# Performance work log

Measured on AMD Instinct MI355X. Metric: run time of the kernel, lower is better.

## Reference

```python
import jax, jax.numpy as jnp
import numpy as np

N, D, H, O, E, K = 4096, 512, 1024, 512, 8, 2


def setup_inputs() -> dict:
    key = jax.random.key(0)
    ks = jax.random.split(key, 7)
    s = 0.02
    return {
        "x": jax.random.normal(ks[0], (N, D), dtype=jnp.float32),
        "W1": jax.random.normal(ks[1], (E, D, H), dtype=jnp.float32) * s,
        "b1": jnp.zeros((E, H), dtype=jnp.float32),
        "W2": jax.random.normal(ks[2], (E, H, O), dtype=jnp.float32) * s,
        "b2": jnp.zeros((E, O), dtype=jnp.float32),
        "Wg": jax.random.normal(ks[3], (D, E), dtype=jnp.float32) * s,
        "bg": jnp.zeros((E,), dtype=jnp.float32),
        "k": K,
    }


def reference(x, W1, b1, W2, b2, Wg, bg, k):
    # Gating: softmax over experts, then top-k with renormalized weights
    gates = jax.nn.softmax(x @ Wg + bg, axis=1)              # [N, E]
    topv, topi = jax.lax.top_k(gates, k)                     # [N, k]
    w = topv / jnp.sum(topv, axis=1, keepdims=True)          # renormalized top-k weights

    # Dense per-expert two-layer MLP (grouped GEMM form)
    h = jax.nn.relu(jnp.einsum('nd,edh->neh', x, W1) + b1[None])   # [N, E, H]
    y = jnp.einsum('neh,eho->neo', h, W2) + b2[None]               # [N, E, O]

    # Gather selected experts and combine
    y_sel = jnp.take_along_axis(y, topi[:, :, None], axis=1)       # [N, k, O]
    out = jnp.einsum('nko,nk->no', y_sel, w)                       # [N, O]
    return out, gates, topi
```

## Files before the change

### kernel.cpp

```cpp
#include <hip/hip_runtime.h>
#include <hip/hip_bf16.h>

#define N_TOK 4096
#define DIM   512
#define HID   1024
#define OUTD  512
#define NEXP  8
#define TOPK  2

#define MT1 72
#define HROWS 9216

typedef __bf16 bf16;
typedef bf16  bf16x8 __attribute__((ext_vector_type(8)));
typedef bf16  bf16x4 __attribute__((ext_vector_type(4)));
typedef float f32x4  __attribute__((ext_vector_type(4)));

__device__ inline f32x4 mfma16(bf16x8 a, bf16x8 b, f32x4 c) {
    return __builtin_amdgcn_mfma_f32_16x16x32_bf16(a, b, c, 0, 0, 0);
}

__device__ inline void gload16(const bf16* g, char* l) {
    __builtin_amdgcn_global_load_lds(
        (const __attribute__((address_space(1))) void*)g,
        (__attribute__((address_space(3))) void*)l, 16, 0, 0);
}

__global__ __launch_bounds__(256) void prep_gate_kernel(
    const float* __restrict__ W1, const float* __restrict__ W2,
    const float* __restrict__ Wg, const float* __restrict__ bg,
    const float* __restrict__ x,
    bf16* __restrict__ W1t, bf16* __restrict__ W2t,
    bf16* __restrict__ xb,
    float* __restrict__ gates_out, float* __restrict__ topi_out,
    int* __restrict__ pick_e, float* __restrict__ pick_w)
{
    __shared__ __align__(16) float smem[NEXP * DIM];
    int b = blockIdx.x;

    if (b >= 8192) {
        const float4* Wg4 = (const float4*)Wg;
        for (int i = threadIdx.x; i < DIM * NEXP / 4; i += 256) {
            float4 v = Wg4[i];
#pragma unroll
            for (int j = 0; j < 4; ++j) {
                int idx = i * 4 + j;
                smem[(idx & 7) * DIM + (idx >> 3)] = ((const float*)&v)[j];
            }
        }
        __syncthreads();

        int wave = threadIdx.x >> 6;
        int lane = threadIdx.x & 63;
        int n = (b - 8192) * 4 + wave;

        const float4* x4 = (const float4*)(x + (size_t)n * DIM);
        float4 v0 = x4[lane];
        float4 v1 = x4[lane + 64];

        bf16x4 o0 = { (bf16)v0.x, (bf16)v0.y, (bf16)v0.z, (bf16)v0.w };
        bf16x4 o1 = { (bf16)v1.x, (bf16)v1.y, (bf16)v1.z, (bf16)v1.w };
        bf16x4* xb4 = (bf16x4*)(xb + (size_t)n * DIM);
        xb4[lane]      = o0;
        xb4[lane + 64] = o1;

        float acc[NEXP];
#pragma unroll
        for (int e = 0; e < NEXP; ++e) {
            const float4* wr = (const float4*)(smem + e * DIM);
            float4 w0 = wr[lane];
            float4 w1 = wr[lane + 64];
            acc[e] = v0.x * w0.x + v0.y * w0.y + v0.z * w0.z + v0.w * w0.w
                   + v1.x * w1.x + v1.y * w1.y + v1.z * w1.z + v1.w * w1.w;
        }
#pragma unroll
        for (int off = 32; off >= 1; off >>= 1) {
#pragma unroll
            for (int e = 0; e < NEXP; ++e) acc[e] += __shfl_xor(acc[e], off, 64);
        }
#pragma unroll
        for (int e = 0; e < NEXP; ++e) acc[e] += bg[e];

        float m = acc[0];
#pragma unroll
        for (int e = 1; e < NEXP; ++e) m = fmaxf(m, acc[e]);
        float g[NEXP];
        float s = 0.f;
#pragma unroll
        for (int e = 0; e < NEXP; ++e) { g[e] = expf(acc[e] - m); s += g[e]; }
        float inv_s = 1.f / s;
#pragma unroll
        for (int e = 0; e < NEXP; ++e) g[e] *= inv_s;

        if (lane < NEXP) gates_out[n * NEXP + lane] = g[lane];

        if (lane == 0) {
            int m1 = 0;
#pragma unroll
            for (int e = 1; e < NEXP; ++e) if (g[e] > g[m1]) m1 = e;
            int m2 = (m1 == 0) ? 1 : 0;
#pragma unroll
            for (int e = 0; e < NEXP; ++e) if (e != m1 && g[e] > g[m2]) m2 = e;
            float v1g = g[m1], v2g = g[m2];
            float inv = 1.f / (v1g + v2g);
            topi_out[n * TOPK + 0] = (float)m1;
            topi_out[n * TOPK + 1] = (float)m2;
            int2 pe = { m1, m2 };
            float2 pw = { v1g * inv, v2g * inv };
            *(int2*)(pick_e + n * 2) = pe;
            *(float2*)(pick_w + n * 2) = pw;
        }
        return;
    }

    float (*tile)[33] = (float(*)[33])smem;
    const float* src; bf16* dst; int R, C, tilex, rem, e;
    if (b < 4096) {
        e = b >> 9; rem = b & 511; R = DIM; C = HID; tilex = 32;
        src = W1; dst = W1t;
    } else {
        b -= 4096;
        e = b >> 9; rem = b & 511; R = HID; C = OUTD; tilex = 16;
        src = W2; dst = W2t;
    }
    const float* s = src + (size_t)e * R * C;
    bf16* d = dst + (size_t)e * R * C;
    int c0 = (rem % tilex) * 32, r0 = (rem / tilex) * 32;

    int tx = threadIdx.x & 31, ty = threadIdx.x >> 5;
#pragma unroll
    for (int i = 0; i < 4; ++i) {
        int r = ty + i * 8;
        tile[r][tx] = s[(size_t)(r0 + r) * C + c0 + tx];
    }
    __syncthreads();

    int t = threadIdx.x;
    int dc = t >> 3, q = t & 7;
    bf16x4 v;
#pragma unroll
    for (int j = 0; j < 4; ++j) v[j] = (bf16)tile[q * 4 + j][dc];
    *(bf16x4*)(d + (size_t)(c0 + dc) * R + r0 + q * 4) = v;
}

__global__ __launch_bounds__(1024) void bucket_sched_kernel(
    const int* __restrict__ pick_e,
    int* __restrict__ counts, int* __restrict__ tlist, int* __restrict__ meta)
{
    __shared__ int cnt[NEXP];
    if (threadIdx.x < NEXP) cnt[threadIdx.x] = 0;
    __syncthreads();
    for (int i = threadIdx.x; i < N_TOK * 2; i += 1024) {
        int e = pick_e[i];
        int p = atomicAdd(&cnt[e], 1);
        tlist[e * N_TOK + p] = i;
    }
    __syncthreads();
    if (threadIdx.x == 0) {
        int base = 0, t1 = 0;
        for (int e = 0; e < NEXP; ++e) {
            int c = cnt[e];
            counts[e] = c;
            int n1 = (c + 127) >> 7;
            for (int lt = 0; lt < n1; ++lt) {
                meta[2 + t1 * 3]     = e;
                meta[2 + t1 * 3 + 1] = base + lt * 128;
                meta[2 + t1 * 3 + 2] = lt * 128;
                ++t1;
            }
            base += n1 << 7;
        }
        meta[0] = t1;
    }
}


__global__ __launch_bounds__(256, 4) void l1_kernel(
    const bf16* __restrict__ xb, const bf16* __restrict__ W1t,
    const float* __restrict__ b1, const int* __restrict__ counts,
    const int* __restrict__ tlist, const int* __restrict__ meta,
    bf16* __restrict__ h)
{
    int mt = blockIdx.x >> 3, nt = blockIdx.x & 7;
    if (mt >= meta[0]) return;
    const int* s1 = meta + 2 + mt * 3;
    int e = s1[0], rb = s1[1], i0 = s1[2];
    int cnt = counts[e];

    __shared__ __align__(16) char lds[32768];

    int tid = threadIdx.x, w = tid >> 6, l = tid & 63;
    int c0 = w * 128 + l, c1 = c0 + 64;
    int rA0 = c0 >> 2, rA1 = c1 >> 2;
    int kA0 = (c0 & 3) ^ ((rA0 & 3) ^ ((rA0 >> 2) & 1));
    int kA1 = (c1 & 3) ^ ((rA1 & 3) ^ ((rA1 >> 2) & 1));
    int iA0 = i0 + rA0, iA1 = i0 + rA1;
    const int* tl = tlist + e * N_TOK;
    int tok0 = iA0 < cnt ? (tl[iA0] >> 1) : 0;
    int tok1 = iA1 < cnt ? (tl[iA1] >> 1) : 0;
    const bf16* sA0 = xb + (size_t)tok0 * DIM + kA0 * 8;
    const bf16* sA1 = xb + (size_t)tok1 * DIM + kA1 * 8;
    int n0 = nt * 128;
    const bf16* w1e = W1t + (size_t)e * HID * DIM;
    const bf16* sB0 = w1e + (size_t)(n0 + rA0) * DIM + kA0 * 8;
    const bf16* sB1 = w1e + (size_t)(n0 + rA1) * DIM + kA1 * 8;
    int oA0 = c0 * 16, oA1 = c1 * 16;

    f32x4 acc[4][4];
#pragma unroll
    for (int mf = 0; mf < 4; ++mf)
#pragma unroll
        for (int nf = 0; nf < 4; ++nf) acc[mf][nf] = (f32x4){0.f, 0.f, 0.f, 0.f};

    int wm = w >> 1, wn = w & 1;
    int lr = l & 15;
    int kb = ((l >> 4) ^ ((l & 3) ^ ((l >> 2) & 1))) * 16;

    {
        char* A = lds;       char* B = lds + 8192;
        gload16(sA0, A + oA0); gload16(sA1, A + oA1);
        gload16(sB0, B + oA0); gload16(sB1, B + oA1);
    }

    for (int ks = 0; ks < 16; ++ks) {
        __syncthreads();
        if (ks < 15) {
            char* A = lds + (((ks + 1) & 1) * 16384);
            char* B = A + 8192;
            int kof = (ks + 1) * 32;
            gload16(sA0 + kof, A + oA0); gload16(sA1 + kof, A + oA1);
            gload16(sB0 + kof, B + oA0); gload16(sB1 + kof, B + oA1);
        }
        char* A = lds + ((ks & 1) * 16384);
        char* B = A + 8192;
        bf16x8 af[4], bfr[4];
#pragma unroll
        for (int mf = 0; mf < 4; ++mf)
            af[mf] = *(const bf16x8*)(A + (wm * 64 + mf * 16 + lr) * 64 + kb);
#pragma unroll
        for (int nf = 0; nf < 4; ++nf)
            bfr[nf] = *(const bf16x8*)(B + (wn * 64 + nf * 16 + lr) * 64 + kb);
#pragma unroll
        for (int mf = 0; mf < 4; ++mf)
#pragma unroll
            for (int nf = 0; nf < 4; ++nf)
                acc[mf][nf] = mfma16(af[mf], bfr[nf], acc[mf][nf]);
    }

    __syncthreads();
    bf16* ct = (bf16*)lds;
    const float* b1e = b1 + e * HID;
#pragma unroll
    for (int nf = 0; nf < 4; ++nf) {
        int col = wn * 64 + nf * 16 + lr;
        float bias = b1e[n0 + col];
#pragma unroll
        for (int mf = 0; mf < 4; ++mf) {
#pragma unroll
            for (int r = 0; r < 4; ++r) {
                int row = wm * 64 + mf * 16 + (l >> 4) * 4 + r;
                float v = fmaxf(acc[mf][nf][r] + bias, 0.f);
                int g = (col >> 3) ^ (row & 3);
                ct[row * 128 + g * 8 + (col & 7)] = (bf16)v;
            }
        }
    }
    __syncthreads();
#pragma unroll
    for (int p = 0; p < 8; ++p) {
        int row = p * 16 + (tid >> 4);
        int ch = tid & 15;
        int g = ch ^ (row & 3);
        bf16x8 v = *(const bf16x8*)(ct + row * 128 + g * 8);
        *(bf16x8*)(h + (size_t)(rb + row) * HID + n0 + ch * 8) = v;
    }
}

__global__ __launch_bounds__(256, 4) void l2_kernel(
    const bf16* __restrict__ h, const bf16* __restrict__ W2t,
    const int* __restrict__ counts, const int* __restrict__ tlist,
    const int* __restrict__ meta, bf16* __restrict__ ybuf)
{
    int mt = blockIdx.x >> 2, nt = blockIdx.x & 3;
    if (mt >= meta[0]) return;
    const int* s1 = meta + 2 + mt * 3;
    int e = s1[0], rb = s1[1], i0 = s1[2];
    int cnt = counts[e];

    __shared__ __align__(16) char lds[32768];

    int tid = threadIdx.x, w = tid >> 6, l = tid & 63;
    int c0 = w * 128 + l, c1 = c0 + 64;
    int rA0 = c0 >> 2, rA1 = c1 >> 2;
    int kA0 = (c0 & 3) ^ ((rA0 & 3) ^ ((rA0 >> 2) & 1));
    int kA1 = (c1 & 3) ^ ((rA1 & 3) ^ ((rA1 >> 2) & 1));
    const bf16* sA0 = h + (size_t)(rb + rA0) * HID + kA0 * 8;
    const bf16* sA1 = h + (size_t)(rb + rA1) * HID + kA1 * 8;
    int n0 = nt * 128;
    const bf16* w2e = W2t + (size_t)e * OUTD * HID;
    const bf16* sB0 = w2e + (size_t)(n0 + rA0) * HID + kA0 * 8;
    const bf16* sB1 = w2e + (size_t)(n0 + rA1) * HID + kA1 * 8;
    int oA0 = c0 * 16, oA1 = c1 * 16;

    f32x4 acc[4][4];
#pragma unroll
    for (int mf = 0; mf < 4; ++mf)
#pragma unroll
        for (int nf = 0; nf < 4; ++nf) acc[mf][nf] = (f32x4){0.f, 0.f, 0.f, 0.f};

    int wm = w >> 1, wn = w & 1;
    int lr = l & 15;
    int kb = ((l >> 4) ^ ((l & 3) ^ ((l >> 2) & 1))) * 16;

    {
        char* A = lds;       char* B = lds + 8192;
        gload16(sA0, A + oA0); gload16(sA1, A + oA1);
        gload16(sB0, B + oA0); gload16(sB1, B + oA1);
    }

    for (int ks = 0; ks < 32; ++ks) {
        __syncthreads();
        if (ks < 31) {
            char* A = lds + (((ks + 1) & 1) * 16384);
            char* B = A + 8192;
            int kof = (ks + 1) * 32;
            gload16(sA0 + kof, A + oA0); gload16(sA1 + kof, A + oA1);
            gload16(sB0 + kof, B + oA0); gload16(sB1 + kof, B + oA1);
        }
        char* A = lds + ((ks & 1) * 16384);
        char* B = A + 8192;
        bf16x8 af[4], bfr[4];
#pragma unroll
        for (int mf = 0; mf < 4; ++mf)
            af[mf] = *(const bf16x8*)(A + (wm * 64 + mf * 16 + lr) * 64 + kb);
#pragma unroll
        for (int nf = 0; nf < 4; ++nf)
            bfr[nf] = *(const bf16x8*)(B + (wn * 64 + nf * 16 + lr) * 64 + kb);
#pragma unroll
        for (int mf = 0; mf < 4; ++mf)
#pragma unroll
            for (int nf = 0; nf < 4; ++nf)
                acc[mf][nf] = mfma16(af[mf], bfr[nf], acc[mf][nf]);
    }

    __syncthreads();
    bf16* ct = (bf16*)lds;
#pragma unroll
    for (int nf = 0; nf < 4; ++nf) {
        int col = wn * 64 + nf * 16 + lr;
#pragma unroll
        for (int mf = 0; mf < 4; ++mf) {
#pragma unroll
            for (int r = 0; r < 4; ++r) {
                int row = wm * 64 + mf * 16 + (l >> 4) * 4 + r;
                int g = (col >> 3) ^ (row & 3);
                ct[row * 128 + g * 8 + (col & 7)] = (bf16)acc[mf][nf][r];
            }
        }
    }
    __syncthreads();
    const int* tl = tlist + e * N_TOK;
#pragma unroll
    for (int p = 0; p < 8; ++p) {
        int row = p * 16 + (tid >> 4);
        int i = i0 + row;
        if (i < cnt) {
            int pi = tl[i];
            int ch = tid & 15;
            int g = ch ^ (row & 3);
            bf16x8 v = *(const bf16x8*)(ct + row * 128 + g * 8);
            *(bf16x8*)(ybuf + (size_t)pi * OUTD + n0 + ch * 8) = v;
        }
    }
}

__global__ __launch_bounds__(256) void combine_kernel(
    const bf16* __restrict__ ybuf, const float* __restrict__ b2,
    const int* __restrict__ pick_e, const float* __restrict__ pick_w,
    float* __restrict__ out)
{
    int wave = threadIdx.x >> 6;
    int lane = threadIdx.x & 63;
    int n = blockIdx.x * 4 + wave;

    int e0 = pick_e[n * 2], e1 = pick_e[n * 2 + 1];
    float w0 = pick_w[n * 2], w1 = pick_w[n * 2 + 1];

    const bf16x8* y0 = (const bf16x8*)(ybuf + (size_t)(n * 2) * OUTD);
    const bf16x8* y1 = (const bf16x8*)(ybuf + (size_t)(n * 2 + 1) * OUTD);
    const float4* b20 = (const float4*)(b2 + e0 * OUTD);
    const float4* b21 = (const float4*)(b2 + e1 * OUTD);
    float4* o4 = (float4*)(out + (size_t)n * OUTD);

    bf16x8 a = y0[lane];
    bf16x8 b = y1[lane];
    float4 c0 = b20[lane * 2], c1 = b20[lane * 2 + 1];
    float4 d0 = b21[lane * 2], d1 = b21[lane * 2 + 1];

    float4 r0, r1;
    r0.x = w0 * ((float)a[0] + c0.x) + w1 * ((float)b[0] + d0.x);
    r0.y = w0 * ((float)a[1] + c0.y) + w1 * ((float)b[1] + d0.y);
    r0.z = w0 * ((float)a[2] + c0.z) + w1 * ((float)b[2] + d0.z);
    r0.w = w0 * ((float)a[3] + c0.w) + w1 * ((float)b[3] + d0.w);
    r1.x = w0 * ((float)a[4] + c1.x) + w1 * ((float)b[4] + d1.x);
    r1.y = w0 * ((float)a[5] + c1.y) + w1 * ((float)b[5] + d1.y);
    r1.z = w0 * ((float)a[6] + c1.z) + w1 * ((float)b[6] + d1.z);
    r1.w = w0 * ((float)a[7] + c1.w) + w1 * ((float)b[7] + d1.w);
    o4[lane * 2]     = r0;
    o4[lane * 2 + 1] = r1;
}

extern "C" void kernel_launch(void* const* d_in, const int* in_sizes, int n_in,
                              void* d_out, int out_size, void* d_ws, size_t ws_size,
                              hipStream_t stream)
{
    const float* x  = (const float*)d_in[0];
    const float* W1 = (const float*)d_in[1];
    const float* b1 = (const float*)d_in[2];
    const float* W2 = (const float*)d_in[3];
    const float* b2 = (const float*)d_in[4];
    const float* Wg = (const float*)d_in[5];
    const float* bg = (const float*)d_in[6];

    float* out_f   = (float*)d_out;
    float* gates_o = out_f + (size_t)N_TOK * OUTD;
    float* topi_o  = gates_o + (size_t)N_TOK * NEXP;

    char* ws = (char*)d_ws;
    size_t offW1t = 0;
    size_t offW2t = offW1t + (size_t)NEXP * HID * DIM * 2;
    size_t offXb  = offW2t + (size_t)NEXP * OUTD * HID * 2;
    size_t offH   = offXb + (size_t)N_TOK * DIM * 2;
    size_t offYb  = offH + (size_t)HROWS * HID * 2;
    size_t offCnt = offYb + (size_t)N_TOK * 2 * OUTD * 2;
    size_t offTl  = offCnt + 256;
    size_t offMeta = offTl + (size_t)NEXP * N_TOK * 4;
    size_t offPkE = offMeta + 4096;
    size_t offPkW = offPkE + (size_t)N_TOK * 2 * 4;

    bf16*  W1t    = (bf16*)(ws + offW1t);
    bf16*  W2t    = (bf16*)(ws + offW2t);
    bf16*  xbuf   = (bf16*)(ws + offXb);
    bf16*  hbuf   = (bf16*)(ws + offH);
    bf16*  ybuf   = (bf16*)(ws + offYb);
    int*   cnts   = (int*)(ws + offCnt);
    int*   tlist  = (int*)(ws + offTl);
    int*   meta   = (int*)(ws + offMeta);
    int*   pick_e = (int*)(ws + offPkE);
    float* pick_w = (float*)(ws + offPkW);

    prep_gate_kernel<<<8192 + N_TOK / 4, 256, 0, stream>>>(
        W1, W2, Wg, bg, x, W1t, W2t, xbuf, gates_o, topi_o, pick_e, pick_w);

    bucket_sched_kernel<<<1, 1024, 0, stream>>>(pick_e, cnts, tlist, meta);

    l1_kernel<<<MT1 * 8, 256, 0, stream>>>(xbuf, W1t, b1, cnts, tlist, meta, hbuf);
    l2_kernel<<<MT1 * 4, 256, 0, stream>>>(hbuf, W2t, cnts, tlist, meta, ybuf);

    combine_kernel<<<N_TOK / 4, 256, 0, stream>>>(ybuf, b2, pick_e, pick_w, out_f);
}
```

Baseline: 77.18 us.

## Fuse L1, L2 and combine kernels into one launch with per-tile flag dependencies

Merges the layer-1 GEMM, layer-2 GEMM and combine kernels into a single launch with block ranges assigned to each stage. L2 blocks spin on per-m-tile completion counters set by the L1 blocks, and combine blocks wait on a global L2-done counter. This removes two kernel launch boundaries and lets L2 tiles start as soon as their own h rows are ready, at the cost of spin-waiting blocks holding CU slots. It relies on dispatch order to avoid deadlock when waiting blocks occupy resources before their producers are scheduled.

```diff
diff --git a/kernel.cpp b/kernel.cpp
--- a/kernel.cpp
+++ b/kernel.cpp
@@ -10,6 +10,9 @@
 
 #define MT1 72
 #define HROWS 9216
+#define L1B (MT1 * 8)
+#define L2B (MT1 * 4)
+#define CMB (N_TOK / 8)
 
 typedef __bf16 bf16;
 typedef bf16  bf16x8 __attribute__((ext_vector_type(8)));
@@ -24,6 +27,13 @@
     __builtin_amdgcn_global_load_lds(
         (const __attribute__((address_space(1))) void*)g,
         (__attribute__((address_space(3))) void*)l, 16, 0, 0);
+}
+
+__device__ inline int aload(const int* p) {
+    return __hip_atomic_load(p, __ATOMIC_RELAXED, __HIP_MEMORY_SCOPE_AGENT);
+}
+__device__ inline void aadd(int* p) {
+    __hip_atomic_fetch_add(p, 1, __ATOMIC_RELAXED, __HIP_MEMORY_SCOPE_AGENT);
 }
 
 __global__ __launch_bounds__(256) void prep_gate_kernel(
@@ -145,10 +155,12 @@
 
 __global__ __launch_bounds__(1024) void bucket_sched_kernel(
     const int* __restrict__ pick_e,
-    int* __restrict__ counts, int* __restrict__ tlist, int* __restrict__ meta)
+    int* __restrict__ counts, int* __restrict__ tlist, int* __restrict__ meta,
+    int* __restrict__ flags)
 {
     __shared__ int cnt[NEXP];
     if (threadIdx.x < NEXP) cnt[threadIdx.x] = 0;
+    if (threadIdx.x < MT1 + 1) flags[threadIdx.x] = 0;
     __syncthreads();
     for (int i = threadIdx.x; i < N_TOK * 2; i += 1024) {
         int e = pick_e[i];
@@ -174,240 +186,258 @@
     }
 }
 
-
-__global__ __launch_bounds__(256, 4) void l1_kernel(
+__global__ __launch_bounds__(256, 4) void l1l2c_kernel(
     const bf16* __restrict__ xb, const bf16* __restrict__ W1t,
-    const float* __restrict__ b1, const int* __restrict__ counts,
-    const int* __restrict__ tlist, const int* __restrict__ meta,
-    bf16* __restrict__ h)
+    const bf16* __restrict__ W2t,
+    const float* __restrict__ b1, const float* __restrict__ b2,
+    const int* __restrict__ counts, const int* __restrict__ tlist,
+    const int* __restrict__ meta,
+    const int* __restrict__ pick_e, const float* __restrict__ pick_w,
+    bf16* __restrict__ h, bf16* __restrict__ ybuf,
+    float* __restrict__ out, int* __restrict__ flags)
 {
-    int mt = blockIdx.x >> 3, nt = blockIdx.x & 7;
-    if (mt >= meta[0]) return;
-    const int* s1 = meta + 2 + mt * 3;
-    int e = s1[0], rb = s1[1], i0 = s1[2];
-    int cnt = counts[e];
-
     __shared__ __align__(16) char lds[32768];
-
-    int tid = threadIdx.x, w = tid >> 6, l = tid & 63;
-    int c0 = w * 128 + l, c1 = c0 + 64;
-    int rA0 = c0 >> 2, rA1 = c1 >> 2;
-    int kA0 = (c0 & 3) ^ ((rA0 & 3) ^ ((rA0 >> 2) & 1));
-    int kA1 = (c1 & 3) ^ ((rA1 & 3) ^ ((rA1 >> 2) & 1));
-    int iA0 = i0 + rA0, iA1 = i0 + rA1;
-    const int* tl = tlist + e * N_TOK;
-    int tok0 = iA0 < cnt ? (tl[iA0] >> 1) : 0;
-    int tok1 = iA1 < cnt ? (tl[iA1] >> 1) : 0;
-    const bf16* sA0 = xb + (size_t)tok0 * DIM + kA0 * 8;
-    const bf16* sA1 = xb + (size_t)tok1 * DIM + kA1 * 8;
-    int n0 = nt * 128;
-    const bf16* w1e = W1t + (size_t)e * HID * DIM;
-    const bf16* sB0 = w1e + (size_t)(n0 + rA0) * DIM + kA0 * 8;
-    const bf16* sB1 = w1e + (size_t)(n0 + rA1) * DIM + kA1 * 8;
-    int oA0 = c0 * 16, oA1 = c1 * 16;
-
-    f32x4 acc[4][4];
-#pragma unroll
-    for (int mf = 0; mf < 4; ++mf)
-#pragma unroll
-        for (int nf = 0; nf < 4; ++nf) acc[mf][nf] = (f32x4){0.f, 0.f, 0.f, 0.f};
-
-    int wm = w >> 1, wn = w & 1;
-    int lr = l & 15;
-    int kb = ((l >> 4) ^ ((l & 3) ^ ((l >> 2) & 1))) * 16;
-
-    {
-        char* A = lds;       char* B = lds + 8192;
-        gload16(sA0, A + oA0); gload16(sA1, A + oA1);
-        gload16(sB0, B + oA0); gload16(sB1, B + oA1);
-    }
-
-    for (int ks = 0; ks < 16; ++ks) {
-        __syncthreads();
-        if (ks < 15) {
-            char* A = lds + (((ks + 1) & 1) * 16384);
+    int bid = blockIdx.x, tid = threadIdx.x;
+    int* mtflag = flags;
+    int* l2done = flags + MT1;
+
+    if (bid < L1B) {
+        int mt = bid >> 3, nt = bid & 7;
+        if (mt >= meta[0]) return;
+        const int* s1 = meta + 2 + mt * 3;
+        int e = s1[0], rb = s1[1], i0 = s1[2];
+        int cnt = counts[e];
+
+        int w = tid >> 6, l = tid & 63;
+        int c0 = w * 128 + l, c1 = c0 + 64;
+        int rA0 = c0 >> 2, rA1 = c1 >> 2;
+        int kA0 = (c0 & 3) ^ ((rA0 & 3) ^ ((rA0 >> 2) & 1));
+        int kA1 = (c1 & 3) ^ ((rA1 & 3) ^ ((rA1 >> 2) & 1));
+        int iA0 = i0 + rA0, iA1 = i0 + rA1;
+        const int* tl = tlist + e * N_TOK;
+        int tok0 = iA0 < cnt ? (tl[iA0] >> 1) : 0;
+        int tok1 = iA1 < cnt ? (tl[iA1] >> 1) : 0;
+        const bf16* sA0 = xb + (size_t)tok0 * DIM + kA0 * 8;
+        const bf16* sA1 = xb + (size_t)tok1 * DIM + kA1 * 8;
+        int n0 = nt * 128;
+        const bf16* w1e = W1t + (size_t)e * HID * DIM;
+        const bf16* sB0 = w1e + (size_t)(n0 + rA0) * DIM + kA0 * 8;
+        const bf16* sB1 = w1e + (size_t)(n0 + rA1) * DIM + kA1 * 8;
+        int oA0 = c0 * 16, oA1 = c1 * 16;
+
+        f32x4 acc[4][4];
+#pragma unroll
+        for (int mf = 0; mf < 4; ++mf)
+#pragma unroll
+            for (int nf = 0; nf < 4; ++nf) acc[mf][nf] = (f32x4){0.f, 0.f, 0.f, 0.f};
+
+        int wm = w >> 1, wn = w & 1;
+        int lr = l & 15;
+        int kb = ((l >> 4) ^ ((l & 3) ^ ((l >> 2) & 1))) * 16;
+
+        {
+            char* A = lds;       char* B = lds + 8192;
+            gload16(sA0, A + oA0); gload16(sA1, A + oA1);
+            gload16(sB0, B + oA0); gload16(sB1, B + oA1);
+        }
+        for (int ks = 0; ks < 16; ++ks) {
+            __syncthreads();
+            if (ks < 15) {
+                char* A = lds + (((ks + 1) & 1) * 16384);
+                char* B = A + 8192;
+                int kof = (ks + 1) * 32;
+                gload16(sA0 + kof, A + oA0); gload16(sA1 + kof, A + oA1);
+                gload16(sB0 + kof, B + oA0); gload16(sB1 + kof, B + oA1);
+            }
+            char* A = lds + ((ks & 1) * 16384);
             char* B = A + 8192;
-            int kof = (ks + 1) * 32;
-            gload16(sA0 + kof, A + oA0); gload16(sA1 + kof, A + oA1);
-            gload16(sB0 + kof, B + oA0); gload16(sB1 + kof, B + oA1);
-        }
-        char* A = lds + ((ks & 1) * 16384);
-        char* B = A + 8192;
-        bf16x8 af[4], bfr[4];
-#pragma unroll
-        for (int mf = 0; mf < 4; ++mf)
-            af[mf] = *(const bf16x8*)(A + (wm * 64 + mf * 16 + lr) * 64 + kb);
-#pragma unroll
-        for (int nf = 0; nf < 4; ++nf)
-            bfr[nf] = *(const bf16x8*)(B + (wn * 64 + nf * 16 + lr) * 64 + kb);
-#pragma unroll
-        for (int mf = 0; mf < 4; ++mf)
+            bf16x8 af[4], bfr[4];
+#pragma unroll
+            for (int mf = 0; mf < 4; ++mf)
+                af[mf] = *(const bf16x8*)(A + (wm * 64 + mf * 16 + lr) * 64 + kb);
 #pragma unroll
             for (int nf = 0; nf < 4; ++nf)
-                acc[mf][nf] = mfma16(af[mf], bfr[nf], acc[mf][nf]);
-    }
-
-    __syncthreads();
-    bf16* ct = (bf16*)lds;
-    const float* b1e = b1 + e * HID;
-#pragma unroll
-    for (int nf = 0; nf < 4; ++nf) {
-        int col = wn * 64 + nf * 16 + lr;
-        float bias = b1e[n0 + col];
-#pragma unroll
-        for (int mf = 0; mf < 4; ++mf) {
-#pragma unroll
-            for (int r = 0; r < 4; ++r) {
-                int row = wm * 64 + mf * 16 + (l >> 4) * 4 + r;
-                float v = fmaxf(acc[mf][nf][r] + bias, 0.f);
-                int g = (col >> 3) ^ (row & 3);
-                ct[row * 128 + g * 8 + (col & 7)] = (bf16)v;
-            }
-        }
-    }
-    __syncthreads();
-#pragma unroll
-    for (int p = 0; p < 8; ++p) {
-        int row = p * 16 + (tid >> 4);
-        int ch = tid & 15;
-        int g = ch ^ (row & 3);
-        bf16x8 v = *(const bf16x8*)(ct + row * 128 + g * 8);
-        *(bf16x8*)(h + (size_t)(rb + row) * HID + n0 + ch * 8) = v;
-    }
-}
-
-__global__ __launch_bounds__(256, 4) void l2_kernel(
-    const bf16* __restrict__ h, const bf16* __restrict__ W2t,
-    const int* __restrict__ counts, const int* __restrict__ tlist,
-    const int* __restrict__ meta, bf16* __restrict__ ybuf)
-{
-    int mt = blockIdx.x >> 2, nt = blockIdx.x & 3;
-    if (mt >= meta[0]) return;
-    const int* s1 = meta + 2 + mt * 3;
-    int e = s1[0], rb = s1[1], i0 = s1[2];
-    int cnt = counts[e];
-
-    __shared__ __align__(16) char lds[32768];
-
-    int tid = threadIdx.x, w = tid >> 6, l = tid & 63;
-    int c0 = w * 128 + l, c1 = c0 + 64;
-    int rA0 = c0 >> 2, rA1 = c1 >> 2;
-    int kA0 = (c0 & 3) ^ ((rA0 & 3) ^ ((rA0 >> 2) & 1));
-    int kA1 = (c1 & 3) ^ ((rA1 & 3) ^ ((rA1 >> 2) & 1));
-    const bf16* sA0 = h + (size_t)(rb + rA0) * HID + kA0 * 8;
-    const bf16* sA1 = h + (size_t)(rb + rA1) * HID + kA1 * 8;
-    int n0 = nt * 128;
-    const bf16* w2e = W2t + (size_t)e * OUTD * HID;
-    const bf16* sB0 = w2e + (size_t)(n0 + rA0) * HID + kA0 * 8;
-    const bf16* sB1 = w2e + (size_t)(n0 + rA1) * HID + kA1 * 8;
-    int oA0 = c0 * 16, oA1 = c1 * 16;
-
-    f32x4 acc[4][4];
-#pragma unroll
-    for (int mf = 0; mf < 4; ++mf)
-#pragma unroll
-        for (int nf = 0; nf < 4; ++nf) acc[mf][nf] = (f32x4){0.f, 0.f, 0.f, 0.f};
-
-    int wm = w >> 1, wn = w & 1;
-    int lr = l & 15;
-    int kb = ((l >> 4) ^ ((l & 3) ^ ((l >> 2) & 1))) * 16;
-
-    {
-        char* A = lds;       char* B = lds + 8192;
-        gload16(sA0, A + oA0); gload16(sA1, A + oA1);
-        gload16(sB0, B + oA0); gload16(sB1, B + oA1);
-    }
-
-    for (int ks = 0; ks < 32; ++ks) {
-        __syncthreads();
-        if (ks < 31) {
-            char* A = lds + (((ks + 1) & 1) * 16384);
-            char* B = A + 8192;
-            int kof = (ks + 1) * 32;
-            gload16(sA0 + kof, A + oA0); gload16(sA1 + kof, A + oA1);
-            gload16(sB0 + kof, B + oA0); gload16(sB1 + kof, B + oA1);
-        }
-        char* A = lds + ((ks & 1) * 16384);
-        char* B = A + 8192;
-        bf16x8 af[4], bfr[4];
-#pragma unroll
-        for (int mf = 0; mf < 4; ++mf)
-            af[mf] = *(const bf16x8*)(A + (wm * 64 + mf * 16 + lr) * 64 + kb);
-#pragma unroll
-        for (int nf = 0; nf < 4; ++nf)
-            bfr[nf] = *(const bf16x8*)(B + (wn * 64 + nf * 16 + lr) * 64 + kb);
-#pragma unroll
-        for (int mf = 0; mf < 4; ++mf)
-#pragma unroll
-            for (int nf = 0; nf < 4; ++nf)
-                acc[mf][nf] = mfma16(af[mf], bfr[nf], acc[mf][nf]);
-    }
-
-    __syncthreads();
-    bf16* ct = (bf16*)lds;
-#pragma unroll
-    for (int nf = 0; nf < 4; ++nf) {
-        int col = wn * 64 + nf * 16 + lr;
-#pragma unroll
-        for (int mf = 0; mf < 4; ++mf) {
-#pragma unroll
-            for (int r = 0; r < 4; ++r) {
-                int row = wm * 64 + mf * 16 + (l >> 4) * 4 + r;
-                int g = (col >> 3) ^ (row & 3);
-                ct[row * 128 + g * 8 + (col & 7)] = (bf16)acc[mf][nf][r];
-            }
-        }
-    }
-    __syncthreads();
-    const int* tl = tlist + e * N_TOK;
-#pragma unroll
-    for (int p = 0; p < 8; ++p) {
-        int row = p * 16 + (tid >> 4);
-        int i = i0 + row;
-        if (i < cnt) {
-            int pi = tl[i];
+                bfr[nf] = *(const bf16x8*)(B + (wn * 64 + nf * 16 + lr) * 64 + kb);
+#pragma unroll
+            for (int mf = 0; mf < 4; ++mf)
+#pragma unroll
+                for (int nf = 0; nf < 4; ++nf)
+                    acc[mf][nf] = mfma16(af[mf], bfr[nf], acc[mf][nf]);
+        }
+
+        __syncthreads();
+        bf16* ct = (bf16*)lds;
+        const float* b1e = b1 + e * HID;
+#pragma unroll
+        for (int nf = 0; nf < 4; ++nf) {
+            int col = wn * 64 + nf * 16 + lr;
+            float bias = b1e[n0 + col];
+#pragma unroll
+            for (int mf = 0; mf < 4; ++mf) {
+#pragma unroll
+                for (int r = 0; r < 4; ++r) {
+                    int row = wm * 64 + mf * 16 + (l >> 4) * 4 + r;
+                    float v = fmaxf(acc[mf][nf][r] + bias, 0.f);
+                    int g = (col >> 3) ^ (row & 3);
+                    ct[row * 128 + g * 8 + (col & 7)] = (bf16)v;
+                }
+            }
+        }
+        __syncthreads();
+#pragma unroll
+        for (int p = 0; p < 8; ++p) {
+            int row = p * 16 + (tid >> 4);
             int ch = tid & 15;
             int g = ch ^ (row & 3);
             bf16x8 v = *(const bf16x8*)(ct + row * 128 + g * 8);
-            *(bf16x8*)(ybuf + (size_t)pi * OUTD + n0 + ch * 8) = v;
-        }
-    }
-}
-
-__global__ __launch_bounds__(256) void combine_kernel(
-    const bf16* __restrict__ ybuf, const float* __restrict__ b2,
-    const int* __restrict__ pick_e, const float* __restrict__ pick_w,
-    float* __restrict__ out)
-{
-    int wave = threadIdx.x >> 6;
-    int lane = threadIdx.x & 63;
-    int n = blockIdx.x * 4 + wave;
-
-    int e0 = pick_e[n * 2], e1 = pick_e[n * 2 + 1];
-    float w0 = pick_w[n * 2], w1 = pick_w[n * 2 + 1];
-
-    const bf16x8* y0 = (const bf16x8*)(ybuf + (size_t)(n * 2) * OUTD);
-    const bf16x8* y1 = (const bf16x8*)(ybuf + (size_t)(n * 2 + 1) * OUTD);
-    const float4* b20 = (const float4*)(b2 + e0 * OUTD);
-    const float4* b21 = (const float4*)(b2 + e1 * OUTD);
-    float4* o4 = (float4*)(out + (size_t)n * OUTD);
-
-    bf16x8 a = y0[lane];
-    bf16x8 b = y1[lane];
-    float4 c0 = b20[lane * 2], c1 = b20[lane * 2 + 1];
-    float4 d0 = b21[lane * 2], d1 = b21[lane * 2 + 1];
-
-    float4 r0, r1;
-    r0.x = w0 * ((float)a[0] + c0.x) + w1 * ((float)b[0] + d0.x);
-    r0.y = w0 * ((float)a[1] + c0.y) + w1 * ((float)b[1] + d0.y);
-    r0.z = w0 * ((float)a[2] + c0.z) + w1 * ((float)b[2] + d0.z);
-    r0.w = w0 * ((float)a[3] + c0.w) + w1 * ((float)b[3] + d0.w);
-    r1.x = w0 * ((float)a[4] + c1.x) + w1 * ((float)b[4] + d1.x);
-    r1.y = w0 * ((float)a[5] + c1.y) + w1 * ((float)b[5] + d1.y);
-    r1.z = w0 * ((float)a[6] + c1.z) + w1 * ((float)b[6] + d1.z);
-    r1.w = w0 * ((float)a[7] + c1.w) + w1 * ((float)b[7] + d1.w);
-    o4[lane * 2]     = r0;
-    o4[lane * 2 + 1] = r1;
+            *(bf16x8*)(h + (size_t)(rb + row) * HID + n0 + ch * 8) = v;
+        }
+        __syncthreads();
+        if (tid == 0) { __threadfence(); aadd(&mtflag[mt]); }
+        return;
+    }
+
+    if (bid < L1B + L2B) {
+        int t = bid - L1B;
+        int mt = t >> 2, nt = t & 3;
+        if (mt >= meta[0]) return;
+        const int* s1 = meta + 2 + mt * 3;
+        int e = s1[0], rb = s1[1], i0 = s1[2];
+        int cnt = counts[e];
+
+        if (tid == 0) {
+            while (aload(&mtflag[mt]) < 8) __builtin_amdgcn_s_sleep(2);
+            __threadfence();
+        }
+        __syncthreads();
+
+        int w = tid >> 6, l = tid & 63;
+        int c0 = w * 128 + l, c1 = c0 + 64;
+        int rA0 = c0 >> 2, rA1 = c1 >> 2;
+        int kA0 = (c0 & 3) ^ ((rA0 & 3) ^ ((rA0 >> 2) & 1));
+        int kA1 = (c1 & 3) ^ ((rA1 & 3) ^ ((rA1 >> 2) & 1));
+        const bf16* sA0 = h + (size_t)(rb + rA0) * HID + kA0 * 8;
+        const bf16* sA1 = h + (size_t)(rb + rA1) * HID + kA1 * 8;
+        int n0 = nt * 128;
+        const bf16* w2e = W2t + (size_t)e * OUTD * HID;
+        const bf16* sB0 = w2e + (size_t)(n0 + rA0) * HID + kA0 * 8;
+        const bf16* sB1 = w2e + (size_t)(n0 + rA1) * HID + kA1 * 8;
+        int oA0 = c0 * 16, oA1 = c1 * 16;
+
+        f32x4 acc[4][4];
+#pragma unroll
+        for (int mf = 0; mf < 4; ++mf)
+#pragma unroll
+            for (int nf = 0; nf < 4; ++nf) acc[mf][nf] = (f32x4){0.f, 0.f, 0.f, 0.f};
+
+        int wm = w >> 1, wn = w & 1;
+        int lr = l & 15;
+        int kb = ((l >> 4) ^ ((l & 3) ^ ((l >> 2) & 1))) * 16;
+
+        {
+            char* A = lds;       char* B = lds + 8192;
+            gload16(sA0, A + oA0); gload16(sA1, A + oA1);
+            gload16(sB0, B + oA0); gload16(sB1, B + oA1);
+        }
+        for (int ks = 0; ks < 32; ++ks) {
+            __syncthreads();
+            if (ks < 31) {
+                char* A = lds + (((ks + 1) & 1) * 16384);
+                char* B = A + 8192;
+                int kof = (ks + 1) * 32;
+                gload16(sA0 + kof, A + oA0); gload16(sA1 + kof, A + oA1);
+                gload16(sB0 + kof, B + oA0); gload16(sB1 + kof, B + oA1);
+            }
+            char* A = lds + ((ks & 1) * 16384);
+            char* B = A + 8192;
+            bf16x8 af[4], bfr[4];
+#pragma unroll
+            for (int mf = 0; mf < 4; ++mf)
+                af[mf] = *(const bf16x8*)(A + (wm * 64 + mf * 16 + lr) * 64 + kb);
+#pragma unroll
+            for (int nf = 0; nf < 4; ++nf)
+                bfr[nf] = *(const bf16x8*)(B + (wn * 64 + nf * 16 + lr) * 64 + kb);
+#pragma unroll
+            for (int mf = 0; mf < 4; ++mf)
+#pragma unroll
+                for (int nf = 0; nf < 4; ++nf)
+                    acc[mf][nf] = mfma16(af[mf], bfr[nf], acc[mf][nf]);
+        }
+
+        __syncthreads();
+        bf16* ct = (bf16*)lds;
+#pragma unroll
+        for (int nf = 0; nf < 4; ++nf) {
+            int col = wn * 64 + nf * 16 + lr;
+#pragma unroll
+            for (int mf = 0; mf < 4; ++mf) {
+#pragma unroll
+                for (int r = 0; r < 4; ++r) {
+                    int row = wm * 64 + mf * 16 + (l >> 4) * 4 + r;
+                    int g = (col >> 3) ^ (row & 3);
+                    ct[row * 128 + g * 8 + (col & 7)] = (bf16)acc[mf][nf][r];
+                }
+            }
+        }
+        __syncthreads();
+        const int* tl = tlist + e * N_TOK;
+#pragma unroll
+        for (int p = 0; p < 8; ++p) {
+            int row = p * 16 + (tid >> 4);
+            int i = i0 + row;
+            if (i < cnt) {
+                int pi = tl[i];
+                int ch = tid & 15;
+                int g = ch ^ (row & 3);
+                bf16x8 v = *(const bf16x8*)(ct + row * 128 + g * 8);
+                *(bf16x8*)(ybuf + (size_t)pi * OUTD + n0 + ch * 8) = v;
+            }
+        }
+        __syncthreads();
+        if (tid == 0) { __threadfence(); aadd(l2done); }
+        return;
+    }
+
+    {
+        int cb = bid - L1B - L2B;
+        if (tid == 0) {
+            int tgt = meta[0] * 4;
+            while (aload(l2done) < tgt) __builtin_amdgcn_s_sleep(2);
+            __threadfence();
+        }
+        __syncthreads();
+
+        int w = tid >> 6, l = tid & 63;
+#pragma unroll
+        for (int j = 0; j < 2; ++j) {
+            int n = cb * 8 + w * 2 + j;
+            int e0 = pick_e[n * 2], e1 = pick_e[n * 2 + 1];
+            float w0 = pick_w[n * 2], w1 = pick_w[n * 2 + 1];
+
+            const bf16x8* y0 = (const bf16x8*)(ybuf + (size_t)(n * 2) * OUTD);
+            const bf16x8* y1 = (const bf16x8*)(ybuf + (size_t)(n * 2 + 1) * OUTD);
+            const float4* b20 = (const float4*)(b2 + e0 * OUTD);
+            const float4* b21 = (const float4*)(b2 + e1 * OUTD);
+            float4* o4 = (float4*)(out + (size_t)n * OUTD);
+
+            bf16x8 a = y0[l];
+            bf16x8 b = y1[l];
+            float4 c0 = b20[l * 2], c1 = b20[l * 2 + 1];
+            float4 d0 = b21[l * 2], d1 = b21[l * 2 + 1];
+
+            float4 r0, r1;
+            r0.x = w0 * ((float)a[0] + c0.x) + w1 * ((float)b[0] + d0.x);
+            r0.y = w0 * ((float)a[1] + c0.y) + w1 * ((float)b[1] + d0.y);
+            r0.z = w0 * ((float)a[2] + c0.z) + w1 * ((float)b[2] + d0.z);
+            r0.w = w0 * ((float)a[3] + c0.w) + w1 * ((float)b[3] + d0.w);
+            r1.x = w0 * ((float)a[4] + c1.x) + w1 * ((float)b[4] + d1.x);
+            r1.y = w0 * ((float)a[5] + c1.y) + w1 * ((float)b[5] + d1.y);
+            r1.z = w0 * ((float)a[6] + c1.z) + w1 * ((float)b[6] + d1.z);
+            r1.w = w0 * ((float)a[7] + c1.w) + w1 * ((float)b[7] + d1.w);
+            o4[l * 2]     = r0;
+            o4[l * 2 + 1] = r1;
+        }
+    }
 }
 
 extern "C" void kernel_launch(void* const* d_in, const int* in_sizes, int n_in,
@@ -437,6 +467,7 @@
     size_t offMeta = offTl + (size_t)NEXP * N_TOK * 4;
     size_t offPkE = offMeta + 4096;
     size_t offPkW = offPkE + (size_t)N_TOK * 2 * 4;
+    size_t offFlg = offPkW + (size_t)N_TOK * 2 * 4;
 
     bf16*  W1t    = (bf16*)(ws + offW1t);
     bf16*  W2t    = (bf16*)(ws + offW2t);
@@ -448,14 +479,14 @@
     int*   meta   = (int*)(ws + offMeta);
     int*   pick_e = (int*)(ws + offPkE);
     float* pick_w = (float*)(ws + offPkW);
+    int*   flags  = (int*)(ws + offFlg);
 
     prep_gate_kernel<<<8192 + N_TOK / 4, 256, 0, stream>>>(
         W1, W2, Wg, bg, x, W1t, W2t, xbuf, gates_o, topi_o, pick_e, pick_w);
 
-    bucket_sched_kernel<<<1, 1024, 0, stream>>>(pick_e, cnts, tlist, meta);
-
-    l1_kernel<<<MT1 * 8, 256, 0, stream>>>(xbuf, W1t, b1, cnts, tlist, meta, hbuf);
-    l2_kernel<<<MT1 * 4, 256, 0, stream>>>(hbuf, W2t, cnts, tlist, meta, ybuf);
-
-    combine_kernel<<<N_TOK / 4, 256, 0, stream>>>(ybuf, b2, pick_e, pick_w, out_f);
-}
+    bucket_sched_kernel<<<1, 1024, 0, stream>>>(pick_e, cnts, tlist, meta, flags);
+
+    l1l2c_kernel<<<L1B + L2B + CMB, 256, 0, stream>>>(
+        xbuf, W1t, W2t, b1, b2, cnts, tlist, meta, pick_e, pick_w,
+        hbuf, ybuf, out_f, flags);
+}
```

After: 159.2 us. +106.3%, slower.

## Move W2 transpose/convert from prep kernel into layer-1 GEMM launch

Applied to the files above, without the earlier changes.

The W2 fp32-to-bf16 transpose is split out of the first prep kernel and appended as extra blocks of the layer-1 GEMM launch. The first kernel now only does the W1 transpose and gating, so the bucket scheduler and L1 can start sooner, and W2 conversion runs alongside L1 GEMM blocks. The trade-off is that transpose blocks compete with GEMM blocks for CUs. The shared LDS and block scheduling order also affect how much real overlap happens.

```diff
diff --git a/kernel.cpp b/kernel.cpp
--- a/kernel.cpp
+++ b/kernel.cpp
@@ -10,6 +10,7 @@
 
 #define MT1 72
 #define HROWS 9216
+#define L1B (MT1 * 8)
 
 typedef __bf16 bf16;
 typedef bf16  bf16x8 __attribute__((ext_vector_type(8)));
@@ -26,19 +27,33 @@
         (__attribute__((address_space(3))) void*)l, 16, 0, 0);
 }
 
-__global__ __launch_bounds__(256) void prep_gate_kernel(
-    const float* __restrict__ W1, const float* __restrict__ W2,
-    const float* __restrict__ Wg, const float* __restrict__ bg,
-    const float* __restrict__ x,
-    bf16* __restrict__ W1t, bf16* __restrict__ W2t,
-    bf16* __restrict__ xb,
+__device__ inline void transpose32(const float* __restrict__ s, bf16* __restrict__ d,
+                                   int C, int R, int c0, int r0, char* ldsb, int tid)
+{
+    float (*tile)[33] = (float(*)[33])ldsb;
+    int tx = tid & 31, ty = tid >> 5;
+#pragma unroll
+    for (int i = 0; i < 4; ++i)
+        tile[ty + i * 8][tx] = s[(size_t)(r0 + ty + i * 8) * C + c0 + tx];
+    __syncthreads();
+    int dc = tid >> 3, q = tid & 7;
+    bf16x4 v;
+#pragma unroll
+    for (int j = 0; j < 4; ++j) v[j] = (bf16)tile[q * 4 + j][dc];
+    *(bf16x4*)(d + (size_t)(c0 + dc) * R + r0 + q * 4) = v;
+}
+
+__global__ __launch_bounds__(256) void w1gate_kernel(
+    const float* __restrict__ W1, const float* __restrict__ Wg,
+    const float* __restrict__ bg, const float* __restrict__ x,
+    bf16* __restrict__ W1t, bf16* __restrict__ xb,
     float* __restrict__ gates_out, float* __restrict__ topi_out,
     int* __restrict__ pick_e, float* __restrict__ pick_w)
 {
     __shared__ __align__(16) float smem[NEXP * DIM];
     int b = blockIdx.x;
 
-    if (b >= 8192) {
+    if (b >= 4096) {
         const float4* Wg4 = (const float4*)Wg;
         for (int i = threadIdx.x; i < DIM * NEXP / 4; i += 256) {
             float4 v = Wg4[i];
@@ -52,7 +67,7 @@
 
         int wave = threadIdx.x >> 6;
         int lane = threadIdx.x & 63;
-        int n = (b - 8192) * 4 + wave;
+        int n = (b - 4096) * 4 + wave;
 
         const float4* x4 = (const float4*)(x + (size_t)n * DIM);
         float4 v0 = x4[lane];
@@ -113,34 +128,9 @@
         return;
     }
 
-    float (*tile)[33] = (float(*)[33])smem;
-    const float* src; bf16* dst; int R, C, tilex, rem, e;
-    if (b < 4096) {
-        e = b >> 9; rem = b & 511; R = DIM; C = HID; tilex = 32;
-        src = W1; dst = W1t;
-    } else {
-        b -= 4096;
-        e = b >> 9; rem = b & 511; R = HID; C = OUTD; tilex = 16;
-        src = W2; dst = W2t;
-    }
-    const float* s = src + (size_t)e * R * C;
-    bf16* d = dst + (size_t)e * R * C;
-    int c0 = (rem % tilex) * 32, r0 = (rem / tilex) * 32;
-
-    int tx = threadIdx.x & 31, ty = threadIdx.x >> 5;
-#pragma unroll
-    for (int i = 0; i < 4; ++i) {
-        int r = ty + i * 8;
-        tile[r][tx] = s[(size_t)(r0 + r) * C + c0 + tx];
-    }
-    __syncthreads();
-
-    int t = threadIdx.x;
-    int dc = t >> 3, q = t & 7;
-    bf16x4 v;
-#pragma unroll
-    for (int j = 0; j < 4; ++j) v[j] = (bf16)tile[q * 4 + j][dc];
-    *(bf16x4*)(d + (size_t)(c0 + dc) * R + r0 + q * 4) = v;
+    int e = b >> 9, rem = b & 511;
+    transpose32(W1 + (size_t)e * DIM * HID, W1t + (size_t)e * DIM * HID,
+                HID, DIM, (rem & 31) * 32, (rem >> 5) * 32, (char*)smem, threadIdx.x);
 }
 
 __global__ __launch_bounds__(1024) void bucket_sched_kernel(
@@ -179,17 +169,27 @@
     const bf16* __restrict__ xb, const bf16* __restrict__ W1t,
     const float* __restrict__ b1, const int* __restrict__ counts,
     const int* __restrict__ tlist, const int* __restrict__ meta,
-    bf16* __restrict__ h)
-{
-    int mt = blockIdx.x >> 3, nt = blockIdx.x & 7;
+    bf16* __restrict__ h,
+    const float* __restrict__ W2, bf16* __restrict__ W2t)
+{
+    __shared__ __align__(16) char lds[32768];
+    int bid = blockIdx.x, tid = threadIdx.x;
+
+    if (bid >= L1B) {
+        int t = bid - L1B;
+        int e = t >> 9, rem = t & 511;
+        transpose32(W2 + (size_t)e * HID * OUTD, W2t + (size_t)e * HID * OUTD,
+                    OUTD, HID, (rem & 15) * 32, (rem >> 4) * 32, lds, tid);
+        return;
+    }
+
+    int mt = bid >> 3, nt = bid & 7;
     if (mt >= meta[0]) return;
     const int* s1 = meta + 2 + mt * 3;
     int e = s1[0], rb = s1[1], i0 = s1[2];
     int cnt = counts[e];
 
-    __shared__ __align__(16) char lds[32768];
-
-    int tid = threadIdx.x, w = tid >> 6, l = tid & 63;
+    int w = tid >> 6, l = tid & 63;
     int c0 = w * 128 + l, c1 = c0 + 64;
     int rA0 = c0 >> 2, rA1 = c1 >> 2;
     int kA0 = (c0 & 3) ^ ((rA0 & 3) ^ ((rA0 >> 2) & 1));
@@ -449,12 +449,14 @@
     int*   pick_e = (int*)(ws + offPkE);
     float* pick_w = (float*)(ws + offPkW);
 
-    prep_gate_kernel<<<8192 + N_TOK / 4, 256, 0, stream>>>(
-        W1, W2, Wg, bg, x, W1t, W2t, xbuf, gates_o, topi_o, pick_e, pick_w);
+    w1gate_kernel<<<4096 + N_TOK / 4, 256, 0, stream>>>(
+        W1, Wg, bg, x, W1t, xbuf, gates_o, topi_o, pick_e, pick_w);
 
     bucket_sched_kernel<<<1, 1024, 0, stream>>>(pick_e, cnts, tlist, meta);
 
-    l1_kernel<<<MT1 * 8, 256, 0, stream>>>(xbuf, W1t, b1, cnts, tlist, meta, hbuf);
+    l1_kernel<<<L1B + 4096, 256, 0, stream>>>(
+        xbuf, W1t, b1, cnts, tlist, meta, hbuf, W2, W2t);
+
     l2_kernel<<<MT1 * 4, 256, 0, stream>>>(hbuf, W2t, cnts, tlist, meta, ybuf);
 
     combine_kernel<<<N_TOK / 4, 256, 0, stream>>>(ybuf, b2, pick_e, pick_w, out_f);
```

After: 75.40 us. -2.3%, faster.
